# Kernel tuning notes

Measured on AMD Instinct MI355X. Metric: run time of the kernel, lower is better.

Reference implementation:

```python
import jax, jax.numpy as jnp
import numpy as np


def _transition_matrix(durations, max_seq_len):
    # durations: (B, L_enc) int; returns (B, L_enc, L_dec) float32
    rng = jnp.arange(max_seq_len)                         # (L_dec,)
    cs = jnp.cumsum(durations, axis=1)[..., None]         # (B, L_enc, 1)
    mask1 = rng < cs
    # torch .roll(1) without dim flattens -> roll -> reshape; jnp.roll(axis=None) matches
    shifted = jnp.roll(durations, 1)
    shifted = shifted.at[:, 0].set(0)
    cs2 = jnp.cumsum(shifted, axis=1)[..., None]
    mask2 = rng < cs2
    tm = mask1 & (~mask2)
    return tm.astype(jnp.float32)


def setup_inputs() -> dict:
    key = jax.random.key(0)
    k1, k2 = jax.random.split(key)
    B, L_enc, E = 32, 512, 256
    L_dec = 2048
    encoder_output = jax.random.normal(k1, (B, L_enc, E), dtype=jnp.float32)
    durations = jax.random.randint(k2, (B, L_enc), 0, 8, dtype=jnp.int64)
    return {
        "encoder_output": encoder_output,
        "durations": durations,
        "decoder_max_seq_len": L_dec,
    }


def reference(encoder_output, durations, decoder_max_seq_len):
    tm = _transition_matrix(durations, decoder_max_seq_len)   # (B, L_enc, L_dec)
    # bmm(enc^T, tm)^T  ==  einsum over L_enc
    return jnp.einsum("ble,bld->bde", encoder_output, tm)     # (B, L_dec, E)
```

## Files before the change

### kernel.cpp

```cpp
#include <hip/hip_runtime.h>

#define B_    32
#define LENC  512
#define LDEC  2048
#define E4    64
#define TPB   256
#define NWAVE (TPB / 64)
#define ROWS_PER_BLOCK 32
#define ROWS_PER_WAVE  (ROWS_PER_BLOCK / NWAVE)

__global__ __launch_bounds__(TPB) void length_regulator_fused(
    const float4* __restrict__ enc, const int2* __restrict__ dur2,
    float4* __restrict__ out) {
  const int t    = threadIdx.x;
  const int lane = t & 63;
  const int wid  = t >> 6;
  const int b    = blockIdx.y;

  __shared__ int cs[LENC];
  __shared__ int wsum[NWAVE];

  const int2 v = dur2[b * (LENC / 2) + t];
  int x = v.x + v.y;
#pragma unroll
  for (int off = 1; off < 64; off <<= 1) {
    const int y = __shfl_up(x, off, 64);
    if (lane >= off) x += y;
  }
  if (lane == 63) wsum[wid] = x;
  __syncthreads();
  int wo = 0;
#pragma unroll
  for (int w = 0; w < NWAVE; ++w) wo += (w < wid) ? wsum[w] : 0;
  const int ip = x + wo;
  cs[2 * t + 1] = ip;
  cs[2 * t]     = ip - v.y;
  __syncthreads();

  const int total = cs[LENC - 1];
  int d = blockIdx.x * ROWS_PER_BLOCK + wid * ROWS_PER_WAVE;

  int lo = 0, hi = LENC;
  while (lo < hi) {
    const int mid = (lo + hi) >> 1;
    if (cs[mid] <= d) lo = mid + 1; else hi = mid;
  }

  const size_t enc_base = (size_t)b * LENC * E4;
  const size_t out_base = (size_t)b * LDEC * E4;
#pragma unroll
  for (int r = 0; r < ROWS_PER_WAVE; ++r, ++d) {
    while (lo < LENC && cs[lo] <= d) ++lo;
    float4 val = make_float4(0.f, 0.f, 0.f, 0.f);
    if (d < total)
      val = enc[enc_base + (size_t)lo * E4 + lane];
    out[out_base + (size_t)d * E4 + lane] = val;
  }
}

extern "C" void kernel_launch(void* const* d_in, const int* in_sizes, int n_in,
                              void* d_out, int out_size, void* d_ws, size_t ws_size,
                              hipStream_t stream) {
  const float* enc = (const float*)d_in[0];
  const int*   dur = (const int*)d_in[1];

  dim3 grid(LDEC / ROWS_PER_BLOCK, B_);
  length_regulator_fused<<<grid, TPB, 0, stream>>>(
      (const float4*)enc, (const int2*)dur, (float4*)d_out);
}
```

Before: 88.09 us.

## Batch gathers before stores, use nontemporal stores, and widen blocks to 512 threads

Block size grows to 512 threads and 64 rows per block, so each thread now loads one duration and the pairwise int2 scan goes away. Source indices for all rows of a wave are resolved first, then all gathered loads are issued together before any store, which raises memory-level parallelism. Output writes use nontemporal stores to avoid polluting the cache. The costs are more registers per thread and fewer blocks, which means lower occupancy.

```diff
diff --git a/kernel.cpp b/kernel.cpp
--- a/kernel.cpp
+++ b/kernel.cpp
@@ -4,14 +4,16 @@
 #define LENC  512
 #define LDEC  2048
 #define E4    64
-#define TPB   256
+#define TPB   512
 #define NWAVE (TPB / 64)
-#define ROWS_PER_BLOCK 32
+#define ROWS_PER_BLOCK 64
 #define ROWS_PER_WAVE  (ROWS_PER_BLOCK / NWAVE)
 
+typedef float float4n __attribute__((ext_vector_type(4)));
+
 __global__ __launch_bounds__(TPB) void length_regulator_fused(
-    const float4* __restrict__ enc, const int2* __restrict__ dur2,
-    float4* __restrict__ out) {
+    const float4n* __restrict__ enc, const int* __restrict__ dur,
+    float4n* __restrict__ out) {
   const int t    = threadIdx.x;
   const int lane = t & 63;
   const int wid  = t >> 6;
@@ -20,8 +22,8 @@
   __shared__ int cs[LENC];
   __shared__ int wsum[NWAVE];
 
-  const int2 v = dur2[b * (LENC / 2) + t];
-  int x = v.x + v.y;
+  const int v = dur[b * LENC + t];
+  int x = v;
 #pragma unroll
   for (int off = 1; off < 64; off <<= 1) {
     const int y = __shfl_up(x, off, 64);
@@ -32,30 +34,38 @@
   int wo = 0;
 #pragma unroll
   for (int w = 0; w < NWAVE; ++w) wo += (w < wid) ? wsum[w] : 0;
-  const int ip = x + wo;
-  cs[2 * t + 1] = ip;
-  cs[2 * t]     = ip - v.y;
+  cs[t] = x + wo;
   __syncthreads();
 
   const int total = cs[LENC - 1];
-  int d = blockIdx.x * ROWS_PER_BLOCK + wid * ROWS_PER_WAVE;
+  const int d0 = blockIdx.x * ROWS_PER_BLOCK + wid * ROWS_PER_WAVE;
 
   int lo = 0, hi = LENC;
   while (lo < hi) {
     const int mid = (lo + hi) >> 1;
-    if (cs[mid] <= d) lo = mid + 1; else hi = mid;
+    if (cs[mid] <= d0) lo = mid + 1; else hi = mid;
   }
 
-  const size_t enc_base = (size_t)b * LENC * E4;
-  const size_t out_base = (size_t)b * LDEC * E4;
+  int los[ROWS_PER_WAVE];
 #pragma unroll
-  for (int r = 0; r < ROWS_PER_WAVE; ++r, ++d) {
-    while (lo < LENC && cs[lo] <= d) ++lo;
-    float4 val = make_float4(0.f, 0.f, 0.f, 0.f);
-    if (d < total)
-      val = enc[enc_base + (size_t)lo * E4 + lane];
-    out[out_base + (size_t)d * E4 + lane] = val;
+  for (int r = 0; r < ROWS_PER_WAVE; ++r) {
+    while (lo < LENC && cs[lo] <= d0 + r) ++lo;
+    los[r] = lo;
   }
+
+  const size_t enc_base = (size_t)b * LENC * E4 + lane;
+  const size_t out_base = (size_t)b * LDEC * E4 + (size_t)d0 * E4 + lane;
+
+  float4n vals[ROWS_PER_WAVE];
+#pragma unroll
+  for (int r = 0; r < ROWS_PER_WAVE; ++r) {
+    vals[r] = (float4n){0.f, 0.f, 0.f, 0.f};
+    if (d0 + r < total)
+      vals[r] = enc[enc_base + (size_t)los[r] * E4];
+  }
+#pragma unroll
+  for (int r = 0; r < ROWS_PER_WAVE; ++r)
+    __builtin_nontemporal_store(vals[r], &out[out_base + (size_t)r * E4]);
 }
 
 extern "C" void kernel_launch(void* const* d_in, const int* in_sizes, int n_in,
@@ -66,5 +76,5 @@
 
   dim3 grid(LDEC / ROWS_PER_BLOCK, B_);
   length_regulator_fused<<<grid, TPB, 0, stream>>>(
-      (const float4*)enc, (const int2*)dur, (float4*)d_out);
+      (const float4n*)enc, dur, (float4n*)d_out);
 }
```

Result: slower. 104.5 us (+18.6%).
